# Kernel tuning notes

Measured on AMD Instinct MI355X. Metric: run time of the kernel, lower is better.

The kernel has to match this reference:

```python
import jax, jax.numpy as jnp
import numpy as np
from jax import lax

B, H, L, DK = 8, 8, 1024, 64
BN_EPS = 1e-5


def _conv_bn_sm(x, w, b, g, beta, pad):
    # x: [B, H, L] (N=batch, C=h heads as channels, spatial=L)
    y = lax.conv_general_dilated(x, w, (1,), [(pad, pad)], dimension_numbers=("NCH", "OIH", "NCH"))
    y = y + b[None, :, None]
    # BatchNorm1d in training mode: batch stats over (N, L) per channel, biased var
    mu = jnp.mean(y, axis=(0, 2), keepdims=True)
    var = jnp.var(y, axis=(0, 2), keepdims=True)
    y = (y - mu) * (g[None, :, None] / jnp.sqrt(var + BN_EPS)) + beta[None, :, None]
    return jax.nn.softmax(y, axis=-1)


def setup_inputs() -> dict:
    key = jax.random.key(0)
    ks = jax.random.split(key, 20)
    n = lambda i, shape, s=1.0: jax.random.normal(ks[i], shape, dtype=jnp.float32) * s
    inp = {
        "Q": n(0, (B, H, L, DK)),
        "K": n(1, (B, H, L, DK)),
        "V": n(2, (B, H, L, DK)),
        "attn_mask": jnp.ones((1,), dtype=bool),
        # proj_q / proj_k: Linear(d_k, 1, bias=False) weight [1, d_k] -> stored as [d_k]
        "wq": n(3, (DK,), 0.1), "wk": n(4, (DK,), 0.1),
        # proj_back_q / proj_back_k: Linear(1, d_k, bias=False) weight [d_k, 1] -> [d_k]
        "wbq": n(5, (DK,), 0.1), "wbk": n(6, (DK,), 0.1),
        # Conv1d(h, h, f) weights [out=h, in=h, f] + bias [h]
        "cq3_w": n(7, (H, H, 3), 0.2), "cq3_b": n(8, (H,), 0.05),
        "cq9_w": n(9, (H, H, 9), 0.1), "cq9_b": n(10, (H,), 0.05),
        "ck3_w": n(11, (H, H, 3), 0.2), "ck3_b": n(12, (H,), 0.05),
        "ck9_w": n(13, (H, H, 9), 0.1), "ck9_b": n(14, (H,), 0.05),
        # BatchNorm1d affine params
        "bnq3_g": jnp.ones((H,), jnp.float32), "bnq3_b": jnp.zeros((H,), jnp.float32),
        "bnq9_g": jnp.ones((H,), jnp.float32), "bnq9_b": jnp.zeros((H,), jnp.float32),
        "bnk3_g": jnp.ones((H,), jnp.float32), "bnk3_b": jnp.zeros((H,), jnp.float32),
        "bnk9_g": jnp.ones((H,), jnp.float32), "bnk9_b": jnp.zeros((H,), jnp.float32),
    }
    return inp


def reference(Q, K, V, attn_mask, wq, wk, wbq, wbk,
              cq3_w, cq3_b, cq9_w, cq9_b, ck3_w, ck3_b, ck9_w, ck9_b,
              bnq3_g, bnq3_b, bnq9_g, bnq9_b, bnk3_g, bnk3_b, bnk9_g, bnk9_b):
    b, h, l, d_k = Q.shape
    l_k = K.shape[2]
    # proj to scalar per position, reshape to [b, h, l]
    Qp = jnp.einsum("bhld,d->bhl", Q, wq)
    Kp = jnp.einsum("bhld,d->bhl", K, wk)
    # multi-scale conv + BN(train) + softmax branches
    q0 = _conv_bn_sm(Qp, cq3_w, cq3_b, bnq3_g, bnq3_b, 1)
    q1 = _conv_bn_sm(Qp, cq9_w, cq9_b, bnq9_g, bnq9_b, 4)
    k0 = _conv_bn_sm(Kp, ck3_w, ck3_b, bnk3_g, bnk3_b, 1)
    k1 = _conv_bn_sm(Kp, ck9_w, ck9_b, bnk9_g, bnk9_b, 4)
    # faithful to torch: cat along dim 0 then C-order reshape to [b,h,l,2], max over last
    Qm = jnp.max(jnp.concatenate([q0, q1], axis=0).reshape(b, h, l, 2), axis=-1)
    Km = jnp.max(jnp.concatenate([k0, k1], axis=0).reshape(b, h, l_k, 2), axis=-1)
    # proj back 1 -> d_k (no bias): outer with weight vector
    Qn = Qm[..., None] * wbq  # [b,h,l,d_k]
    Kn = Km[..., None] * wbk  # [b,h,l_k,d_k]
    scores = jnp.einsum("bhqd,bhkd->bhqk", Qn, Kn) / jnp.sqrt(jnp.float32(d_k))
    attn = jax.nn.softmax(scores, axis=-1)
    context = jnp.einsum("bhqk,bhkd->bhqd", attn, V)
    return (context, attn)
```

## Files before the change

### kernel.cpp

```cpp
#include <hip/hip_runtime.h>

constexpr int SL = 1024;
constexpr int NBH = 64;

constexpr int QP_OFF = 0;
constexpr int KP_OFF = 65536;
constexpr int Y_OFF  = 131072;
constexpr int QM_OFF = 655360;
constexpr int KM_OFF = 720896;
constexpr int ST_OFF = 786432;
constexpr int C_OFF  = 786496;
constexpr int VT_OFF = 786560;

typedef __attribute__((ext_vector_type(8))) short short8;
typedef __attribute__((ext_vector_type(4))) float f32x4;

__device__ inline unsigned short f2bf(float x) {
    unsigned int u = __float_as_uint(x);
    unsigned int r = (u + 0x7fff + ((u >> 16) & 1)) >> 16;
    return (unsigned short)r;
}

__global__ __launch_bounds__(256) void k_projpack(
    const float* __restrict__ Q, const float* __restrict__ K,
    const float* __restrict__ V,
    const float* __restrict__ wq, const float* __restrict__ wk,
    const float* __restrict__ wbq, const float* __restrict__ wbk,
    float* __restrict__ ws)
{
    int b = blockIdx.x;
    int tid = threadIdx.x;
    if (b < 8192) {
        bool isQ = b < 4096;
        const float* src = isQ ? Q : K;
        const float* w   = isQ ? wq : wk;
        int row = (b - (isQ ? 0 : 4096)) * 16 + (tid >> 4);
        int l16 = tid & 15;
        float4 x  = ((const float4*)(src + row * 64))[l16];
        float4 w4 = ((const float4*)w)[l16];
        float v = x.x * w4.x + x.y * w4.y + x.z * w4.z + x.w * w4.w;
        #pragma unroll
        for (int m = 8; m; m >>= 1) v += __shfl_xor(v, m);
        if (l16 == 0) ws[(isQ ? QP_OFF : KP_OFF) + row] = v;
    } else if (b < 10240) {
        int t = (b - 8192) * 256 + tid;
        int lane = t & 63;
        int s    = (t >> 6) & 7;
        int dsub = (t >> 9) & 3;
        int chunk= (t >> 11) & 3;
        int bh   = t >> 13;
        const float* vb = V + bh * (SL * 64);
        int k0 = chunk * 256 + s * 32 + (lane >> 4) * 8;
        int d  = dsub * 16 + (lane & 15);
        unsigned short o[8];
        #pragma unroll
        for (int j = 0; j < 8; j++) o[j] = f2bf(vb[(k0 + j) * 64 + d]);
        unsigned short* vt = (unsigned short*)(ws + VT_OFF);
        *(short8*)(vt + (size_t)t * 8) = *(short8*)o;
    } else {
        if (tid < 64) {
            ws[ST_OFF + tid] = 0.f;
            float v = wbq[tid] * wbk[tid];
            #pragma unroll
            for (int m = 32; m; m >>= 1) v += __shfl_xor(v, m);
            if (tid == 0) ws[C_OFF] = v * 0.125f;
        }
    }
}

__global__ __launch_bounds__(256) void k_conv(
    float* __restrict__ ws,
    const float* __restrict__ w0, const float* __restrict__ b0,
    const float* __restrict__ w1, const float* __restrict__ b1,
    const float* __restrict__ w2, const float* __restrict__ b2,
    const float* __restrict__ w3, const float* __restrict__ b3)
{
    int branch = blockIdx.x >> 6;
    int n = (blockIdx.x >> 3) & 7;
    int seg = blockIdx.x & 7;
    int t0 = seg * 128;
    const float* wp = branch == 0 ? w0 : branch == 1 ? w1 : branch == 2 ? w2 : w3;
    const float* bp = branch == 0 ? b0 : branch == 1 ? b1 : branch == 2 ? b2 : b3;
    const int F = (branch & 1) ? 9 : 3;
    const int PAD = F >> 1;
    const float* x = ws + ((branch < 2) ? QP_OFF : KP_OFF) + n * 8 * SL;

    __shared__ float xl[8][136];
    __shared__ float wl[8 * 8 * 9];
    __shared__ float bl[8];
    int tid = threadIdx.x;
    for (int i = tid; i < 8 * 8 * F; i += 256) wl[i] = wp[i];
    if (tid < 8) bl[tid] = bp[tid];
    for (int i = tid; i < 8 * 136; i += 256) {
        int ci = i / 136; int tt = i - ci * 136;
        int ta = t0 + tt - 4;
        xl[ci][tt] = (ta >= 0 && ta < SL) ? x[ci * SL + ta] : 0.f;
    }
    __syncthreads();
    int c = tid >> 5, u = tid & 31;
    float s1 = 0.f, s2 = 0.f;
    float* yout = ws + Y_OFF + branch * (NBH * SL) + (n * 8 + c) * SL + t0;
    #pragma unroll
    for (int q = 0; q < 4; q++) {
        int tl = q * 32 + u;
        float acc = bl[c];
        for (int ci = 0; ci < 8; ci++) {
            const float* xr = &xl[ci][tl + 4 - PAD];
            const float* wr = &wl[(c * 8 + ci) * F];
            for (int f = 0; f < F; f++) acc += wr[f] * xr[f];
        }
        yout[tl] = acc;
        s1 += acc; s2 += acc * acc;
    }
    #pragma unroll
    for (int m = 16; m; m >>= 1) {
        s1 += __shfl_xor(s1, m);
        s2 += __shfl_xor(s2, m);
    }
    if (u == 0) {
        atomicAdd(&ws[ST_OFF + (branch * 8 + c) * 2],     s1);
        atomicAdd(&ws[ST_OFF + (branch * 8 + c) * 2 + 1], s2);
    }
}

__global__ __launch_bounds__(256) void k_bnmix(
    float* __restrict__ ws,
    const float* __restrict__ g0, const float* __restrict__ be0,
    const float* __restrict__ g1, const float* __restrict__ be1,
    const float* __restrict__ g2, const float* __restrict__ be2,
    const float* __restrict__ g3, const float* __restrict__ be3)
{
    int blk = blockIdx.x;
    int which = blk >> 6;
    int i = (blk >> 3) & 7, j = blk & 7;
    int n = 2 * i + (j >= 4 ? 1 : 0);
    int br = which * 2 + (n >= 8 ? 1 : 0);
    int row = n & 7;
    int tid = threadIdx.x;
    int half = tid >> 7;
    int u = tid & 127;
    int c = 2 * (j & 3) + half;
    const float* gp = br == 0 ? g0 : br == 1 ? g1 : br == 2 ? g2 : g3;
    const float* bp = br == 0 ? be0 : br == 1 ? be1 : br == 2 ? be2 : be3;
    float s1 = ws[ST_OFF + (br * 8 + c) * 2];
    float s2 = ws[ST_OFF + (br * 8 + c) * 2 + 1];
    float mu  = s1 * (1.f / 8192.f);
    float var = s2 * (1.f / 8192.f) - mu * mu;
    float sc = gp[c] * rsqrtf(var + 1e-5f);
    float sh = bp[c] - mu * sc;
    const float* y = ws + Y_OFF + br * (NBH * SL) + (row * 8 + c) * SL;
    float4 ya = ((const float4*)y)[u * 2];
    float4 yb = ((const float4*)y)[u * 2 + 1];
    float z[8] = { ya.x * sc + sh, ya.y * sc + sh, ya.z * sc + sh, ya.w * sc + sh,
                   yb.x * sc + sh, yb.y * sc + sh, yb.z * sc + sh, yb.w * sc + sh };
    float mx = z[0];
    #pragma unroll
    for (int q = 1; q < 8; q++) mx = fmaxf(mx, z[q]);
    __shared__ float r1[4], r2[4];
    #pragma unroll
    for (int m = 32; m; m >>= 1) mx = fmaxf(mx, __shfl_xor(mx, m));
    if ((tid & 63) == 0) r1[tid >> 6] = mx;
    __syncthreads();
    mx = half ? fmaxf(r1[2], r1[3]) : fmaxf(r1[0], r1[1]);
    float e[8];
    float s = 0.f;
    #pragma unroll
    for (int q = 0; q < 8; q++) { e[q] = __expf(z[q] - mx); s += e[q]; }
    #pragma unroll
    for (int m = 32; m; m >>= 1) s += __shfl_xor(s, m);
    if ((tid & 63) == 0) r2[tid >> 6] = s;
    __syncthreads();
    s = half ? (r2[2] + r2[3]) : (r2[0] + r2[1]);
    float inv = 1.f / s;
    float4 o = make_float4(fmaxf(e[0], e[1]) * inv, fmaxf(e[2], e[3]) * inv,
                           fmaxf(e[4], e[5]) * inv, fmaxf(e[6], e[7]) * inv);
    float* outp = ws + (which ? KM_OFF : QM_OFF) + i * 8192 + j * 1024 + half * 512;
    ((float4*)outp)[u] = o;
}

__global__ __launch_bounds__(256, 4) void k_attn(
    float* __restrict__ out, const float* __restrict__ ws)
{
    int p = blockIdx.x;
    int xcd = p & 7, idx = p >> 3;
    int bh = xcd + 8 * (idx >> 5);
    int qt2 = idx & 31;
    int tid = threadIdx.x;

    __shared__ __align__(16) float kml[1024];
    __shared__ float rmx[4], rmn[4];
    __shared__ float wsum0[4][16], wsum1[4][16];
    __shared__ float accred[4][16][64];

    const float* km = ws + KM_OFF + bh * SL;
    const float* qm = ws + QM_OFF + bh * SL + qt2 * 32;
    float c = ws[C_OFF];

    float lmax = -1e30f, lmin = 1e30f;
    #pragma unroll
    for (int i = 0; i < 4; i++) {
        float v = km[tid + 256 * i];
        kml[tid + 256 * i] = v;
        lmax = fmaxf(lmax, v); lmin = fminf(lmin, v);
    }
    #pragma unroll
    for (int m = 32; m; m >>= 1) {
        lmax = fmaxf(lmax, __shfl_xor(lmax, m));
        lmin = fminf(lmin, __shfl_xor(lmin, m));
    }
    if ((tid & 63) == 0) { rmx[tid >> 6] = lmax; rmn[tid >> 6] = lmin; }
    __syncthreads();

    int w = tid >> 6, lane = tid & 63;
    int m16 = lane & 15, kg = lane >> 4;
    float kmax = fmaxf(fmaxf(rmx[0], rmx[1]), fmaxf(rmx[2], rmx[3]));
    float kmin = fminf(fminf(rmn[0], rmn[1]), fminf(rmn[2], rmn[3]));
    float a0 = c * qm[m16];
    float a1 = c * qm[16 + m16];
    float mm0 = (a0 > 0.f) ? a0 * kmax : a0 * kmin;
    float mm1 = (a1 > 0.f) ? a1 * kmax : a1 * kmin;

    float rs0 = 0.f, rs1 = 0.f;
    #pragma unroll
    for (int s = 0; s < 8; s++) {
        const float4* kp = (const float4*)(kml + w * 256 + s * 32 + kg * 8);
        float4 ka = kp[0], kb = kp[1];
        rs0 += __expf(a0 * ka.x - mm0); rs1 += __expf(a1 * ka.x - mm1);
        rs0 += __expf(a0 * ka.y - mm0); rs1 += __expf(a1 * ka.y - mm1);
        rs0 += __expf(a0 * ka.z - mm0); rs1 += __expf(a1 * ka.z - mm1);
        rs0 += __expf(a0 * ka.w - mm0); rs1 += __expf(a1 * ka.w - mm1);
        rs0 += __expf(a0 * kb.x - mm0); rs1 += __expf(a1 * kb.x - mm1);
        rs0 += __expf(a0 * kb.y - mm0); rs1 += __expf(a1 * kb.y - mm1);
        rs0 += __expf(a0 * kb.z - mm0); rs1 += __expf(a1 * kb.z - mm1);
        rs0 += __expf(a0 * kb.w - mm0); rs1 += __expf(a1 * kb.w - mm1);
    }
    rs0 += __shfl_xor(rs0, 16); rs0 += __shfl_xor(rs0, 32);
    rs1 += __shfl_xor(rs1, 16); rs1 += __shfl_xor(rs1, 32);
    if (lane < 16) { wsum0[w][lane] = rs0; wsum1[w][lane] = rs1; }
    __syncthreads();
    float rr0 = 1.f / (wsum0[0][m16] + wsum0[1][m16] + wsum0[2][m16] + wsum0[3][m16]);
    float rr1 = 1.f / (wsum1[0][m16] + wsum1[1][m16] + wsum1[2][m16] + wsum1[3][m16]);

    float* attn_row0 = out + 4194304 + ((size_t)(bh * SL + qt2 * 32 + m16)) * SL;
    float* attn_row1 = attn_row0 + (size_t)16 * SL;
    const short8* vt8 = (const short8*)((const unsigned short*)(ws + VT_OFF))
                        + (size_t)bh * 8192 + w * 2048;

    f32x4 p0a = {0,0,0,0}, p0b = {0,0,0,0}, p0c = {0,0,0,0}, p0d = {0,0,0,0};
    f32x4 p1a = {0,0,0,0}, p1b = {0,0,0,0}, p1c = {0,0,0,0}, p1d = {0,0,0,0};

    #pragma unroll
    for (int s = 0; s < 8; s++) {
        int k0 = w * 256 + s * 32 + kg * 8;
        const float4* kp = (const float4*)(kml + k0);
        float4 ka = kp[0], kb = kp[1];
        const short8* bbase = vt8 + s * 64 + lane;
        short8 b0 = bbase[0 * 512];
        short8 b1 = bbase[1 * 512];
        short8 b2 = bbase[2 * 512];
        short8 b3 = bbase[3 * 512];
        {
            float es[8];
            es[0] = __expf(a0 * ka.x - mm0) * rr0;
            es[1] = __expf(a0 * ka.y - mm0) * rr0;
            es[2] = __expf(a0 * ka.z - mm0) * rr0;
            es[3] = __expf(a0 * ka.w - mm0) * rr0;
            es[4] = __expf(a0 * kb.x - mm0) * rr0;
            es[5] = __expf(a0 * kb.y - mm0) * rr0;
            es[6] = __expf(a0 * kb.z - mm0) * rr0;
            es[7] = __expf(a0 * kb.w - mm0) * rr0;
            *(float4*)(attn_row0 + k0)     = make_float4(es[0], es[1], es[2], es[3]);
            *(float4*)(attn_row0 + k0 + 4) = make_float4(es[4], es[5], es[6], es[7]);
            unsigned short af[8];
            #pragma unroll
            for (int j = 0; j < 8; j++) af[j] = f2bf(es[j]);
            short8 av = *(short8*)af;
            p0a = __builtin_amdgcn_mfma_f32_16x16x32_bf16(av, b0, p0a, 0, 0, 0);
            p0b = __builtin_amdgcn_mfma_f32_16x16x32_bf16(av, b1, p0b, 0, 0, 0);
            p0c = __builtin_amdgcn_mfma_f32_16x16x32_bf16(av, b2, p0c, 0, 0, 0);
            p0d = __builtin_amdgcn_mfma_f32_16x16x32_bf16(av, b3, p0d, 0, 0, 0);
        }
        {
            float es[8];
            es[0] = __expf(a1 * ka.x - mm1) * rr1;
            es[1] = __expf(a1 * ka.y - mm1) * rr1;
            es[2] = __expf(a1 * ka.z - mm1) * rr1;
            es[3] = __expf(a1 * ka.w - mm1) * rr1;
            es[4] = __expf(a1 * kb.x - mm1) * rr1;
            es[5] = __expf(a1 * kb.y - mm1) * rr1;
            es[6] = __expf(a1 * kb.z - mm1) * rr1;
            es[7] = __expf(a1 * kb.w - mm1) * rr1;
            *(float4*)(attn_row1 + k0)     = make_float4(es[0], es[1], es[2], es[3]);
            *(float4*)(attn_row1 + k0 + 4) = make_float4(es[4], es[5], es[6], es[7]);
            unsigned short af[8];
            #pragma unroll
            for (int j = 0; j < 8; j++) af[j] = f2bf(es[j]);
            short8 av = *(short8*)af;
            p1a = __builtin_amdgcn_mfma_f32_16x16x32_bf16(av, b0, p1a, 0, 0, 0);
            p1b = __builtin_amdgcn_mfma_f32_16x16x32_bf16(av, b1, p1b, 0, 0, 0);
            p1c = __builtin_amdgcn_mfma_f32_16x16x32_bf16(av, b2, p1c, 0, 0, 0);
            p1d = __builtin_amdgcn_mfma_f32_16x16x32_bf16(av, b3, p1d, 0, 0, 0);
        }
    }

    #pragma unroll
    for (int reg = 0; reg < 4; reg++) {
        int r = kg * 4 + reg;
        accred[w][r][ 0 + m16] = p0a[reg];
        accred[w][r][16 + m16] = p0b[reg];
        accred[w][r][32 + m16] = p0c[reg];
        accred[w][r][48 + m16] = p0d[reg];
    }
    __syncthreads();
    {
        int r  = tid >> 4;
        int d0 = (tid & 15) * 4;
        float4 s0 = *(const float4*)&accred[0][r][d0];
        float4 s1 = *(const float4*)&accred[1][r][d0];
        float4 s2 = *(const float4*)&accred[2][r][d0];
        float4 s3 = *(const float4*)&accred[3][r][d0];
        float4 o = make_float4(s0.x + s1.x + s2.x + s3.x,
                               s0.y + s1.y + s2.y + s3.y,
                               s0.z + s1.z + s2.z + s3.z,
                               s0.w + s1.w + s2.w + s3.w);
        float* ctx = out + ((size_t)(bh * SL + qt2 * 32 + r)) * 64 + d0;
        *(float4*)ctx = o;
    }
    __syncthreads();
    #pragma unroll
    for (int reg = 0; reg < 4; reg++) {
        int r = kg * 4 + reg;
        accred[w][r][ 0 + m16] = p1a[reg];
        accred[w][r][16 + m16] = p1b[reg];
        accred[w][r][32 + m16] = p1c[reg];
        accred[w][r][48 + m16] = p1d[reg];
    }
    __syncthreads();
    {
        int r  = tid >> 4;
        int d0 = (tid & 15) * 4;
        float4 s0 = *(const float4*)&accred[0][r][d0];
        float4 s1 = *(const float4*)&accred[1][r][d0];
        float4 s2 = *(const float4*)&accred[2][r][d0];
        float4 s3 = *(const float4*)&accred[3][r][d0];
        float4 o = make_float4(s0.x + s1.x + s2.x + s3.x,
                               s0.y + s1.y + s2.y + s3.y,
                               s0.z + s1.z + s2.z + s3.z,
                               s0.w + s1.w + s2.w + s3.w);
        float* ctx = out + ((size_t)(bh * SL + qt2 * 32 + 16 + r)) * 64 + d0;
        *(float4*)ctx = o;
    }
}

extern "C" void kernel_launch(void* const* d_in, const int* in_sizes, int n_in,
                              void* d_out, int out_size, void* d_ws, size_t ws_size,
                              hipStream_t stream)
{
    const float* Q      = (const float*)d_in[0];
    const float* K      = (const float*)d_in[1];
    const float* V      = (const float*)d_in[2];
    const float* wq     = (const float*)d_in[4];
    const float* wk     = (const float*)d_in[5];
    const float* wbq    = (const float*)d_in[6];
    const float* wbk    = (const float*)d_in[7];
    const float* cq3_w  = (const float*)d_in[8];
    const float* cq3_b  = (const float*)d_in[9];
    const float* cq9_w  = (const float*)d_in[10];
    const float* cq9_b  = (const float*)d_in[11];
    const float* ck3_w  = (const float*)d_in[12];
    const float* ck3_b  = (const float*)d_in[13];
    const float* ck9_w  = (const float*)d_in[14];
    const float* ck9_b  = (const float*)d_in[15];
    const float* bnq3_g = (const float*)d_in[16];
    const float* bnq3_b = (const float*)d_in[17];
    const float* bnq9_g = (const float*)d_in[18];
    const float* bnq9_b = (const float*)d_in[19];
    const float* bnk3_g = (const float*)d_in[20];
    const float* bnk3_b = (const float*)d_in[21];
    const float* bnk9_g = (const float*)d_in[22];
    const float* bnk9_b = (const float*)d_in[23];
    float* out = (float*)d_out;
    float* ws  = (float*)d_ws;

    k_projpack<<<10241, 256, 0, stream>>>(Q, K, V, wq, wk, wbq, wbk, ws);
    k_conv<<<256, 256, 0, stream>>>(ws, cq3_w, cq3_b, cq9_w, cq9_b,
                                    ck3_w, ck3_b, ck9_w, ck9_b);
    k_bnmix<<<128, 256, 0, stream>>>(ws, bnq3_g, bnq3_b, bnq9_g, bnq9_b,
                                     bnk3_g, bnk3_b, bnk9_g, bnk9_b);
    k_attn<<<2048, 256, 0, stream>>>(out, ws);
}
```

Baseline: 393.3 us.

## Stage per-head V tile in LDS and loop eight query tiles per block

```diff
diff --git a/kernel.cpp b/kernel.cpp
--- a/kernel.cpp
+++ b/kernel.cpp
@@ -178,13 +178,14 @@
     ((float4*)outp)[u] = o;
 }
 
-__global__ __launch_bounds__(256, 4) void k_attn(
+__global__ void k_attn(
     float* __restrict__ out, const float* __restrict__ ws)
 {
+    extern __shared__ unsigned short bpk[];
     int p = blockIdx.x;
-    int xcd = p & 7, idx = p >> 3;
-    int bh = xcd + 8 * (idx >> 5);
-    int qt2 = idx & 31;
+    int xcd = p & 7, j = p >> 3;
+    int bh = xcd + 8 * (j >> 2);
+    int quarter = j & 3;
     int tid = threadIdx.x;
 
     __shared__ __align__(16) float kml[1024];
@@ -192,10 +193,21 @@
     __shared__ float wsum0[4][16], wsum1[4][16];
     __shared__ float accred[4][16][64];
 
+    {
+        const uint4* src = (const uint4*)((const unsigned short*)(ws + VT_OFF)
+                                          + (size_t)bh * 65536);
+        uint4* dst = (uint4*)bpk;
+        #pragma unroll
+        for (int b = 0; b < 4; ++b) {
+            uint4 tmp[8];
+            #pragma unroll
+            for (int i = 0; i < 8; ++i) tmp[i] = src[tid + 256 * (b * 8 + i)];
+            #pragma unroll
+            for (int i = 0; i < 8; ++i) dst[tid + 256 * (b * 8 + i)] = tmp[i];
+        }
+    }
+
     const float* km = ws + KM_OFF + bh * SL;
-    const float* qm = ws + QM_OFF + bh * SL + qt2 * 32;
-    float c = ws[C_OFF];
-
     float lmax = -1e30f, lmin = 1e30f;
     #pragma unroll
     for (int i = 0; i < 4; i++) {
@@ -215,140 +227,145 @@
     int m16 = lane & 15, kg = lane >> 4;
     float kmax = fmaxf(fmaxf(rmx[0], rmx[1]), fmaxf(rmx[2], rmx[3]));
     float kmin = fminf(fminf(rmn[0], rmn[1]), fminf(rmn[2], rmn[3]));
-    float a0 = c * qm[m16];
-    float a1 = c * qm[16 + m16];
-    float mm0 = (a0 > 0.f) ? a0 * kmax : a0 * kmin;
-    float mm1 = (a1 > 0.f) ? a1 * kmax : a1 * kmin;
-
-    float rs0 = 0.f, rs1 = 0.f;
-    #pragma unroll
-    for (int s = 0; s < 8; s++) {
-        const float4* kp = (const float4*)(kml + w * 256 + s * 32 + kg * 8);
-        float4 ka = kp[0], kb = kp[1];
-        rs0 += __expf(a0 * ka.x - mm0); rs1 += __expf(a1 * ka.x - mm1);
-        rs0 += __expf(a0 * ka.y - mm0); rs1 += __expf(a1 * ka.y - mm1);
-        rs0 += __expf(a0 * ka.z - mm0); rs1 += __expf(a1 * ka.z - mm1);
-        rs0 += __expf(a0 * ka.w - mm0); rs1 += __expf(a1 * ka.w - mm1);
-        rs0 += __expf(a0 * kb.x - mm0); rs1 += __expf(a1 * kb.x - mm1);
-        rs0 += __expf(a0 * kb.y - mm0); rs1 += __expf(a1 * kb.y - mm1);
-        rs0 += __expf(a0 * kb.z - mm0); rs1 += __expf(a1 * kb.z - mm1);
-        rs0 += __expf(a0 * kb.w - mm0); rs1 += __expf(a1 * kb.w - mm1);
-    }
-    rs0 += __shfl_xor(rs0, 16); rs0 += __shfl_xor(rs0, 32);
-    rs1 += __shfl_xor(rs1, 16); rs1 += __shfl_xor(rs1, 32);
-    if (lane < 16) { wsum0[w][lane] = rs0; wsum1[w][lane] = rs1; }
-    __syncthreads();
-    float rr0 = 1.f / (wsum0[0][m16] + wsum0[1][m16] + wsum0[2][m16] + wsum0[3][m16]);
-    float rr1 = 1.f / (wsum1[0][m16] + wsum1[1][m16] + wsum1[2][m16] + wsum1[3][m16]);
-
-    float* attn_row0 = out + 4194304 + ((size_t)(bh * SL + qt2 * 32 + m16)) * SL;
-    float* attn_row1 = attn_row0 + (size_t)16 * SL;
-    const short8* vt8 = (const short8*)((const unsigned short*)(ws + VT_OFF))
-                        + (size_t)bh * 8192 + w * 2048;
-
-    f32x4 p0a = {0,0,0,0}, p0b = {0,0,0,0}, p0c = {0,0,0,0}, p0d = {0,0,0,0};
-    f32x4 p1a = {0,0,0,0}, p1b = {0,0,0,0}, p1c = {0,0,0,0}, p1d = {0,0,0,0};
-
-    #pragma unroll
-    for (int s = 0; s < 8; s++) {
-        int k0 = w * 256 + s * 32 + kg * 8;
-        const float4* kp = (const float4*)(kml + k0);
-        float4 ka = kp[0], kb = kp[1];
-        const short8* bbase = vt8 + s * 64 + lane;
-        short8 b0 = bbase[0 * 512];
-        short8 b1 = bbase[1 * 512];
-        short8 b2 = bbase[2 * 512];
-        short8 b3 = bbase[3 * 512];
+    float c = ws[C_OFF];
+
+    for (int pass = 0; pass < 8; ++pass) {
+        int qt2 = quarter * 8 + pass;
+        const float* qm = ws + QM_OFF + bh * SL + qt2 * 32;
+        float a0 = c * qm[m16];
+        float a1 = c * qm[16 + m16];
+        float mm0 = (a0 > 0.f) ? a0 * kmax : a0 * kmin;
+        float mm1 = (a1 > 0.f) ? a1 * kmax : a1 * kmin;
+
+        float rs0 = 0.f, rs1 = 0.f;
+        #pragma unroll
+        for (int s = 0; s < 8; s++) {
+            const float4* kp = (const float4*)(kml + w * 256 + s * 32 + kg * 8);
+            float4 ka = kp[0], kb = kp[1];
+            rs0 += __expf(a0 * ka.x - mm0); rs1 += __expf(a1 * ka.x - mm1);
+            rs0 += __expf(a0 * ka.y - mm0); rs1 += __expf(a1 * ka.y - mm1);
+            rs0 += __expf(a0 * ka.z - mm0); rs1 += __expf(a1 * ka.z - mm1);
+            rs0 += __expf(a0 * ka.w - mm0); rs1 += __expf(a1 * ka.w - mm1);
+            rs0 += __expf(a0 * kb.x - mm0); rs1 += __expf(a1 * kb.x - mm1);
+            rs0 += __expf(a0 * kb.y - mm0); rs1 += __expf(a1 * kb.y - mm1);
+            rs0 += __expf(a0 * kb.z - mm0); rs1 += __expf(a1 * kb.z - mm1);
+            rs0 += __expf(a0 * kb.w - mm0); rs1 += __expf(a1 * kb.w - mm1);
+        }
+        rs0 += __shfl_xor(rs0, 16); rs0 += __shfl_xor(rs0, 32);
+        rs1 += __shfl_xor(rs1, 16); rs1 += __shfl_xor(rs1, 32);
+        if (lane < 16) { wsum0[w][lane] = rs0; wsum1[w][lane] = rs1; }
+        __syncthreads();
+        float rr0 = 1.f / (wsum0[0][m16] + wsum0[1][m16] + wsum0[2][m16] + wsum0[3][m16]);
+        float rr1 = 1.f / (wsum1[0][m16] + wsum1[1][m16] + wsum1[2][m16] + wsum1[3][m16]);
+
+        float* attn_row0 = out + 4194304 + ((size_t)(bh * SL + qt2 * 32 + m16)) * SL;
+        float* attn_row1 = attn_row0 + (size_t)16 * SL;
+
+        f32x4 p0a = {0,0,0,0}, p0b = {0,0,0,0}, p0c = {0,0,0,0}, p0d = {0,0,0,0};
+        f32x4 p1a = {0,0,0,0}, p1b = {0,0,0,0}, p1c = {0,0,0,0}, p1d = {0,0,0,0};
+
+        #pragma unroll
+        for (int s = 0; s < 8; s++) {
+            int k0 = w * 256 + s * 32 + kg * 8;
+            const float4* kp = (const float4*)(kml + k0);
+            float4 ka = kp[0], kb = kp[1];
+            const short8* bbase = (const short8*)bpk + w * 2048 + s * 64 + lane;
+            short8 b0 = bbase[0 * 512];
+            short8 b1 = bbase[1 * 512];
+            short8 b2 = bbase[2 * 512];
+            short8 b3 = bbase[3 * 512];
+            {
+                float es[8];
+                es[0] = __expf(a0 * ka.x - mm0) * rr0;
+                es[1] = __expf(a0 * ka.y - mm0) * rr0;
+                es[2] = __expf(a0 * ka.z - mm0) * rr0;
+                es[3] = __expf(a0 * ka.w - mm0) * rr0;
+                es[4] = __expf(a0 * kb.x - mm0) * rr0;
+                es[5] = __expf(a0 * kb.y - mm0) * rr0;
+                es[6] = __expf(a0 * kb.z - mm0) * rr0;
+                es[7] = __expf(a0 * kb.w - mm0) * rr0;
+                *(float4*)(attn_row0 + k0)     = make_float4(es[0], es[1], es[2], es[3]);
+                *(float4*)(attn_row0 + k0 + 4) = make_float4(es[4], es[5], es[6], es[7]);
+                unsigned short af[8];
+                #pragma unroll
+                for (int jj = 0; jj < 8; jj++) af[jj] = f2bf(es[jj]);
+                short8 av = *(short8*)af;
+                p0a = __builtin_amdgcn_mfma_f32_16x16x32_bf16(av, b0, p0a, 0, 0, 0);
+                p0b = __builtin_amdgcn_mfma_f32_16x16x32_bf16(av, b1, p0b, 0, 0, 0);
+                p0c = __builtin_amdgcn_mfma_f32_16x16x32_bf16(av, b2, p0c, 0, 0, 0);
+                p0d = __builtin_amdgcn_mfma_f32_16x16x32_bf16(av, b3, p0d, 0, 0, 0);
+            }
+            {
+                float es[8];
+                es[0] = __expf(a1 * ka.x - mm1) * rr1;
+                es[1] = __expf(a1 * ka.y - mm1) * rr1;
+                es[2] = __expf(a1 * ka.z - mm1) * rr1;
+                es[3] = __expf(a1 * ka.w - mm1) * rr1;
+                es[4] = __expf(a1 * kb.x - mm1) * rr1;
+                es[5] = __expf(a1 * kb.y - mm1) * rr1;
+                es[6] = __expf(a1 * kb.z - mm1) * rr1;
+                es[7] = __expf(a1 * kb.w - mm1) * rr1;
+                *(float4*)(attn_row1 + k0)     = make_float4(es[0], es[1], es[2], es[3]);
+                *(float4*)(attn_row1 + k0 + 4) = make_float4(es[4], es[5], es[6], es[7]);
+                unsigned short af[8];
+                #pragma unroll
+                for (int jj = 0; jj < 8; jj++) af[jj] = f2bf(es[jj]);
+                short8 av = *(short8*)af;
+                p1a = __builtin_amdgcn_mfma_f32_16x16x32_bf16(av, b0, p1a, 0, 0, 0);
+                p1b = __builtin_amdgcn_mfma_f32_16x16x32_bf16(av, b1, p1b, 0, 0, 0);
+                p1c = __builtin_amdgcn_mfma_f32_16x16x32_bf16(av, b2, p1c, 0, 0, 0);
+                p1d = __builtin_amdgcn_mfma_f32_16x16x32_bf16(av, b3, p1d, 0, 0, 0);
+            }
+        }
+
+        #pragma unroll
+        for (int reg = 0; reg < 4; reg++) {
+            int r = kg * 4 + reg;
+            accred[w][r][ 0 + m16] = p0a[reg];
+            accred[w][r][16 + m16] = p0b[reg];
+            accred[w][r][32 + m16] = p0c[reg];
+            accred[w][r][48 + m16] = p0d[reg];
+        }
+        __syncthreads();
         {
-            float es[8];
-            es[0] = __expf(a0 * ka.x - mm0) * rr0;
-            es[1] = __expf(a0 * ka.y - mm0) * rr0;
-            es[2] = __expf(a0 * ka.z - mm0) * rr0;
-            es[3] = __expf(a0 * ka.w - mm0) * rr0;
-            es[4] = __expf(a0 * kb.x - mm0) * rr0;
-            es[5] = __expf(a0 * kb.y - mm0) * rr0;
-            es[6] = __expf(a0 * kb.z - mm0) * rr0;
-            es[7] = __expf(a0 * kb.w - mm0) * rr0;
-            *(float4*)(attn_row0 + k0)     = make_float4(es[0], es[1], es[2], es[3]);
-            *(float4*)(attn_row0 + k0 + 4) = make_float4(es[4], es[5], es[6], es[7]);
-            unsigned short af[8];
-            #pragma unroll
-            for (int j = 0; j < 8; j++) af[j] = f2bf(es[j]);
-            short8 av = *(short8*)af;
-            p0a = __builtin_amdgcn_mfma_f32_16x16x32_bf16(av, b0, p0a, 0, 0, 0);
-            p0b = __builtin_amdgcn_mfma_f32_16x16x32_bf16(av, b1, p0b, 0, 0, 0);
-            p0c = __builtin_amdgcn_mfma_f32_16x16x32_bf16(av, b2, p0c, 0, 0, 0);
-            p0d = __builtin_amdgcn_mfma_f32_16x16x32_bf16(av, b3, p0d, 0, 0, 0);
-        }
+            int r  = tid >> 4;
+            int d0 = (tid & 15) * 4;
+            float4 s0 = *(const float4*)&accred[0][r][d0];
+            float4 s1 = *(const float4*)&accred[1][r][d0];
+            float4 s2 = *(const float4*)&accred[2][r][d0];
+            float4 s3 = *(const float4*)&accred[3][r][d0];
+            float4 o = make_float4(s0.x + s1.x + s2.x + s3.x,
+                                   s0.y + s1.y + s2.y + s3.y,
+                                   s0.z + s1.z + s2.z + s3.z,
+                                   s0.w + s1.w + s2.w + s3.w);
+            float* ctx = out + ((size_t)(bh * SL + qt2 * 32 + r)) * 64 + d0;
+            *(float4*)ctx = o;
+        }
+        __syncthreads();
+        #pragma unroll
+        for (int reg = 0; reg < 4; reg++) {
+            int r = kg * 4 + reg;
+            accred[w][r][ 0 + m16] = p1a[reg];
+            accred[w][r][16 + m16] = p1b[reg];
+            accred[w][r][32 + m16] = p1c[reg];
+            accred[w][r][48 + m16] = p1d[reg];
+        }
+        __syncthreads();
         {
-            float es[8];
-            es[0] = __expf(a1 * ka.x - mm1) * rr1;
-            es[1] = __expf(a1 * ka.y - mm1) * rr1;
-            es[2] = __expf(a1 * ka.z - mm1) * rr1;
-            es[3] = __expf(a1 * ka.w - mm1) * rr1;
-            es[4] = __expf(a1 * kb.x - mm1) * rr1;
-            es[5] = __expf(a1 * kb.y - mm1) * rr1;
-            es[6] = __expf(a1 * kb.z - mm1) * rr1;
-            es[7] = __expf(a1 * kb.w - mm1) * rr1;
-            *(float4*)(attn_row1 + k0)     = make_float4(es[0], es[1], es[2], es[3]);
-            *(float4*)(attn_row1 + k0 + 4) = make_float4(es[4], es[5], es[6], es[7]);
-            unsigned short af[8];
-            #pragma unroll
-            for (int j = 0; j < 8; j++) af[j] = f2bf(es[j]);
-            short8 av = *(short8*)af;
-            p1a = __builtin_amdgcn_mfma_f32_16x16x32_bf16(av, b0, p1a, 0, 0, 0);
-            p1b = __builtin_amdgcn_mfma_f32_16x16x32_bf16(av, b1, p1b, 0, 0, 0);
-            p1c = __builtin_amdgcn_mfma_f32_16x16x32_bf16(av, b2, p1c, 0, 0, 0);
-            p1d = __builtin_amdgcn_mfma_f32_16x16x32_bf16(av, b3, p1d, 0, 0, 0);
-        }
-    }
-
-    #pragma unroll
-    for (int reg = 0; reg < 4; reg++) {
-        int r = kg * 4 + reg;
-        accred[w][r][ 0 + m16] = p0a[reg];
-        accred[w][r][16 + m16] = p0b[reg];
-        accred[w][r][32 + m16] = p0c[reg];
-        accred[w][r][48 + m16] = p0d[reg];
-    }
-    __syncthreads();
-    {
-        int r  = tid >> 4;
-        int d0 = (tid & 15) * 4;
-        float4 s0 = *(const float4*)&accred[0][r][d0];
-        float4 s1 = *(const float4*)&accred[1][r][d0];
-        float4 s2 = *(const float4*)&accred[2][r][d0];
-        float4 s3 = *(const float4*)&accred[3][r][d0];
-        float4 o = make_float4(s0.x + s1.x + s2.x + s3.x,
-                               s0.y + s1.y + s2.y + s3.y,
-                               s0.z + s1.z + s2.z + s3.z,
-                               s0.w + s1.w + s2.w + s3.w);
-        float* ctx = out + ((size_t)(bh * SL + qt2 * 32 + r)) * 64 + d0;
-        *(float4*)ctx = o;
-    }
-    __syncthreads();
-    #pragma unroll
-    for (int reg = 0; reg < 4; reg++) {
-        int r = kg * 4 + reg;
-        accred[w][r][ 0 + m16] = p1a[reg];
-        accred[w][r][16 + m16] = p1b[reg];
-        accred[w][r][32 + m16] = p1c[reg];
-        accred[w][r][48 + m16] = p1d[reg];
-    }
-    __syncthreads();
-    {
-        int r  = tid >> 4;
-        int d0 = (tid & 15) * 4;
-        float4 s0 = *(const float4*)&accred[0][r][d0];
-        float4 s1 = *(const float4*)&accred[1][r][d0];
-        float4 s2 = *(const float4*)&accred[2][r][d0];
-        float4 s3 = *(const float4*)&accred[3][r][d0];
-        float4 o = make_float4(s0.x + s1.x + s2.x + s3.x,
-                               s0.y + s1.y + s2.y + s3.y,
-                               s0.z + s1.z + s2.z + s3.z,
-                               s0.w + s1.w + s2.w + s3.w);
-        float* ctx = out + ((size_t)(bh * SL + qt2 * 32 + 16 + r)) * 64 + d0;
-        *(float4*)ctx = o;
+            int r  = tid >> 4;
+            int d0 = (tid & 15) * 4;
+            float4 s0 = *(const float4*)&accred[0][r][d0];
+            float4 s1 = *(const float4*)&accred[1][r][d0];
+            float4 s2 = *(const float4*)&accred[2][r][d0];
+            float4 s3 = *(const float4*)&accred[3][r][d0];
+            float4 o = make_float4(s0.x + s1.x + s2.x + s3.x,
+                                   s0.y + s1.y + s2.y + s3.y,
+                                   s0.z + s1.z + s2.z + s3.z,
+                                   s0.w + s1.w + s2.w + s3.w);
+            float* ctx = out + ((size_t)(bh * SL + qt2 * 32 + 16 + r)) * 64 + d0;
+            *(float4*)ctx = o;
+        }
+        __syncthreads();
     }
 }
 
@@ -387,5 +404,5 @@
                                     ck3_w, ck3_b, ck9_w, ck9_b);
     k_bnmix<<<128, 256, 0, stream>>>(ws, bnq3_g, bnq3_b, bnq9_g, bnq9_b,
                                      bnk3_g, bnk3_b, bnk9_g, bnk9_b);
-    k_attn<<<2048, 256, 0, stream>>>(out, ws);
-}
+    k_attn<<<256, 256, 131072, stream>>>(out, ws);
+}
```

After: 399.9 us. Within noise of the previous version (+1.7%).
